# Optimization experiments

Measured on AMD Instinct MI355X. Metric: run time of the kernel, lower is better.

Reference implementation:

```python
import jax, jax.numpy as jnp
import numpy as np

HEADS = 16
ROPE_BASE = 10000.0


def _rope(x, cos, sin):
    # x: [B, H, L, hd]; rotate_half = [-x2, x1]
    x1, x2 = jnp.split(x, 2, axis=-1)
    rot = jnp.concatenate((-x2, x1), axis=-1)
    return x * cos + rot * sin


def setup_inputs() -> dict:
    key = jax.random.key(0)
    ks = jax.random.split(key, 8)
    B, L, D = 2, 2048, 1024
    s = 0.02
    inp = {
        "Q": jax.random.normal(ks[0], (B, L, D), jnp.float32),
        "K": jax.random.normal(ks[1], (B, L, D), jnp.float32),
        "V": jax.random.normal(ks[2], (B, L, D), jnp.float32),
        # Linear weights stored as [in, out] (transpose of torch's [out, in])
        "Wq": jax.random.normal(ks[3], (D, D), jnp.float32) * s,
        "Wk": jax.random.normal(ks[4], (D, D), jnp.float32) * s,
        "Wv": jax.random.normal(ks[5], (D, D), jnp.float32) * s,
        "Wo": jax.random.normal(ks[6], (D, D), jnp.float32) * s,
        "bq": jnp.zeros((D,), jnp.float32),
        "bk": jnp.zeros((D,), jnp.float32),
        "bv": jnp.zeros((D,), jnp.float32),
        "bo": jnp.zeros((D,), jnp.float32),
        # causal mask, 0 = masked, broadcast to [B,1,L,L]
        "mask": jnp.broadcast_to(jnp.tril(jnp.ones((L, L), jnp.int32))[None, None], (B, 1, L, L)),
    }
    return inp


def reference(Q, K, V, Wq, Wk, Wv, Wo, bq, bk, bv, bo, mask):
    B, L, D = Q.shape
    H = HEADS
    hd = D // H

    def proj(x, W, b):
        # [B,L,D] -> [B,H,L,hd]
        return (x @ W + b).reshape(B, -1, H, hd).transpose(0, 2, 1, 3)

    q = proj(Q, Wq, bq)
    k = proj(K, Wk, bk)
    v = proj(V, Wv, bv)

    # RoPE tables (deterministic constants)
    inv_freq = 1.0 / (ROPE_BASE ** (jnp.arange(0, hd, 2, dtype=jnp.float32) / hd))
    t = jnp.arange(L, dtype=jnp.float32)
    freqs = jnp.outer(t, inv_freq)              # [L, hd/2]
    emb = jnp.concatenate((freqs, freqs), -1)   # [L, hd]
    cos = jnp.cos(emb)[None, None]              # [1,1,L,hd]
    sin = jnp.sin(emb)[None, None]
    q = _rope(q, cos, sin)
    k = _rope(k, cos, sin)

    scale = jnp.sqrt(jnp.asarray(hd, q.dtype))
    scores = jnp.einsum('bhqd,bhkd->bhqk', q, k) / scale
    scores = jnp.where(mask == 0, jnp.asarray(-1e9, scores.dtype), scores)
    attn = jax.nn.softmax(scores, axis=-1)
    out = jnp.einsum('bhqk,bhkd->bhqd', attn, v)
    out = out.transpose(0, 2, 1, 3).reshape(B, L, D)
    return out @ Wo + bo
```

## Files before the change

kernel.cpp:

```cpp
#include <hip/hip_runtime.h>

typedef __attribute__((ext_vector_type(8))) short short8;
typedef __attribute__((ext_vector_type(4))) float f32x4;
typedef unsigned short u16;
typedef unsigned int u32;

#define MFMA_BF16(a, b, c) __builtin_amdgcn_mfma_f32_16x16x32_bf16((a), (b), (c), 0, 0, 0)

constexpr int D = 1024;
constexpr int L = 2048;
constexpr int NHEAD = 16;
constexpr int HD = 64;
constexpr float QLAMBDA = 0.125f * 1.44269504088896340736f;

__device__ __forceinline__ u16 f2bf(float f) {
  unsigned u = __builtin_bit_cast(unsigned, f);
  u = (u + 0x7fffu + ((u >> 16) & 1u)) >> 16;
  return (u16)u;
}

__device__ __forceinline__ short8 cvt8(f32x4 lo, f32x4 hi) {
  short8 r;
  r[0] = (short)f2bf(lo[0]); r[1] = (short)f2bf(lo[1]);
  r[2] = (short)f2bf(lo[2]); r[3] = (short)f2bf(lo[3]);
  r[4] = (short)f2bf(hi[0]); r[5] = (short)f2bf(hi[1]);
  r[6] = (short)f2bf(hi[2]); r[7] = (short)f2bf(hi[3]);
  return r;
}

__device__ __forceinline__ void gload16(const u16* src, u16* dst) {
  __builtin_amdgcn_global_load_lds(
      (const __attribute__((address_space(1))) u32*)(src),
      (__attribute__((address_space(3))) u32*)(dst), 16, 0, 0);
}

__global__ __launch_bounds__(256) void wt_trans_kernel(const float* W0, const float* W1,
                                                       const float* W2, const float* W3,
                                                       u16* out) {
  const float* W = blockIdx.z == 0 ? W0 : blockIdx.z == 1 ? W1 : blockIdx.z == 2 ? W2 : W3;
  u16* o = out + (size_t)blockIdx.z * D * D;
  __shared__ float t[32][33];
  int x = threadIdx.x & 31, y = threadIdx.x >> 5;
  int k0 = blockIdx.x * 32, n0 = blockIdx.y * 32;
#pragma unroll
  for (int i = 0; i < 4; i++) {
    int ky = y * 4 + i;
    t[ky][x] = W[(size_t)(k0 + ky) * D + n0 + x];
  }
  __syncthreads();
#pragma unroll
  for (int i = 0; i < 4; i++) {
    int ny = y * 4 + i;
    o[(size_t)(n0 + ny) * D + k0 + x] = f2bf(t[x][ny]);
  }
}

__global__ __launch_bounds__(256) void rope_tab_kernel(float* ct, float* st) {
  int t = blockIdx.x * 256 + threadIdx.x;
  int i = t & 31, pos = t >> 5;
  float invf = powf(10000.0f, -(float)i / 32.0f);
  float ang = (float)pos * invf;
  ct[t] = cosf(ang);
  st[t] = sinf(ang);
}

__global__ __launch_bounds__(256) void cvt_x_kernel(const float* Q, const float* K,
                                                    const float* V, u16* xb) {
  const float* src = blockIdx.y == 0 ? Q : blockIdx.y == 1 ? K : V;
  u16* dst = xb + (size_t)blockIdx.y * 4096 * D;
  int t = blockIdx.x * 256 + threadIdx.x;
  const float* p = src + (size_t)t * 8;
  f32x4 lo = *(const f32x4*)p;
  f32x4 hi = *(const f32x4*)(p + 4);
  *(short8*)(dst + (size_t)t * 8) = cvt8(lo, hi);
}


__global__ __launch_bounds__(256, 3) void proj_gemm_staged(
    const u16* xb, const u16* wT,
    const float* bq, const float* bk, const float* bv,
    const float* ct, const float* st,
    u16* qo, u16* ko, u16* vT) {
  int i = blockIdx.x;
  int swz = (i & 7) * 96 + (i >> 3);
  int z = swz >> 8;
  int bx = swz & 7;
  int by = (swz >> 3) & 31;

  const u16* A = xb + (size_t)z * 4096 * D;
  const u16* W = wT + (size_t)z * D * D;
  const float* bias = z == 0 ? bq : z == 1 ? bk : bv;

  int w = threadIdx.x >> 6, lane = threadIdx.x & 63;
  int r = lane & 15, c = lane >> 4;
  int wr = w >> 1, wc = w & 1;
  int m0 = by * 128 + wr * 64;
  int n0 = bx * 128 + wc * 64;

  __shared__ __align__(16) u16 lsA[2][4096];
  __shared__ __align__(16) u16 lsB[2][4096];

  const u16* aSrc[2];
  const u16* bSrc[2];
  int dstOff[2];
#pragma unroll
  for (int i2 = 0; i2 < 2; i2++) {
    int q0 = i2 * 256 + w * 64;
    int qq = q0 + lane;
    int t = qq >> 2;
    int gch = (qq & 3) ^ ((t >> 1) & 3);
    aSrc[i2] = A + (size_t)(by * 128 + t) * D + gch * 8;
    bSrc[i2] = W + (size_t)(bx * 128 + t) * D + gch * 8;
    dstOff[i2] = q0 * 8;
  }

  int aOff[4], bOff[4];
#pragma unroll
  for (int mi = 0; mi < 4; mi++) {
    int rowA = wr * 64 + mi * 16 + r;
    aOff[mi] = rowA * 32 + ((c ^ ((rowA >> 1) & 3)) << 3);
    int rowB = wc * 64 + mi * 16 + r;
    bOff[mi] = rowB * 32 + ((c ^ ((rowB >> 1) & 3)) << 3);
  }

  f32x4 acc[4][4];
#pragma unroll
  for (int mi = 0; mi < 4; mi++)
#pragma unroll
    for (int ni = 0; ni < 4; ni++) acc[mi][ni] = f32x4{0.f, 0.f, 0.f, 0.f};

#pragma unroll
  for (int i2 = 0; i2 < 2; i2++) {
    gload16(aSrc[i2], &lsA[0][dstOff[i2]]);
    gload16(bSrc[i2], &lsB[0][dstOff[i2]]);
  }

  auto compute = [&](const u16* pa, const u16* pb) {
    short8 af[4], bf[4];
#pragma unroll
    for (int mi = 0; mi < 4; mi++) af[mi] = *(const short8*)(pa + aOff[mi]);
#pragma unroll
    for (int ni = 0; ni < 4; ni++) bf[ni] = *(const short8*)(pb + bOff[ni]);
#pragma unroll
    for (int mi = 0; mi < 4; mi++)
#pragma unroll
      for (int ni = 0; ni < 4; ni++)
        acc[mi][ni] = MFMA_BF16(af[mi], bf[ni], acc[mi][ni]);
  };

  for (int kt = 0; kt < 31; kt++) {
    int cur = kt & 1;
    __syncthreads();
#pragma unroll
    for (int i2 = 0; i2 < 2; i2++) {
      gload16(aSrc[i2] + (kt + 1) * 32, &lsA[cur ^ 1][dstOff[i2]]);
      gload16(bSrc[i2] + (kt + 1) * 32, &lsB[cur ^ 1][dstOff[i2]]);
    }
    compute(lsA[cur], lsB[cur]);
  }
  __syncthreads();
  compute(lsA[1], lsB[1]);

  int h = n0 >> 6;
#pragma unroll
  for (int mi = 0; mi < 4; mi++) {
#pragma unroll
    for (int j = 0; j < 4; j++) {
      int grow = m0 + mi * 16 + c * 4 + j;
      int b = grow >> 11, ll = grow & 2047;
      if (z < 2) {
        u16* o = (z == 0) ? qo : ko;
        float lam = (z == 0) ? QLAMBDA : 1.0f;
        size_t dst = ((size_t)(b * NHEAD + h) * L + ll) * HD;
#pragma unroll
        for (int ni = 0; ni < 2; ni++) {
          int d = ni * 16 + r;
          float x1 = acc[mi][ni][j] + bias[n0 + d];
          float x2 = acc[mi][ni + 2][j] + bias[n0 + 32 + d];
          float cs = ct[ll * 32 + d], sn = st[ll * 32 + d];
          o[dst + d]      = f2bf((x1 * cs - x2 * sn) * lam);
          o[dst + d + 32] = f2bf((x2 * cs + x1 * sn) * lam);
        }
      } else {
#pragma unroll
        for (int ni = 0; ni < 4; ni++) {
          int d = ni * 16 + r;
          float val = acc[mi][ni][j] + bias[n0 + d];
          vT[((size_t)(b * NHEAD + h) * HD + d) * L + ll] = f2bf(val);
        }
      }
    }
  }
}

__global__ __launch_bounds__(256) void proj_gemm_f32(
    const float* Qf, const float* Kf, const float* Vf, const u16* wT,
    const float* bq, const float* bk, const float* bv,
    const float* ct, const float* st,
    u16* qo, u16* ko, u16* vT) {
  int i = blockIdx.x;
  int swz = (i & 7) * 96 + (i >> 3);
  int z = swz >> 8;
  int bx = swz & 7;
  int by = (swz >> 3) & 31;

  const u16* W = wT + (size_t)z * D * D;
  const float* bias = z == 0 ? bq : z == 1 ? bk : bv;

  int w = threadIdx.x >> 6, lane = threadIdx.x & 63;
  int r = lane & 15, c = lane >> 4;
  int wr = w >> 1, wc = w & 1;
  int m0 = by * 128 + wr * 64;
  int n0 = bx * 128 + wc * 64;

  const float* Af = z == 0 ? Qf : z == 1 ? Kf : Vf;
  const float* a0f = Af + (size_t)(m0 + r) * D + c * 8;
  const u16* b0 = W + (size_t)(n0 + r) * D + c * 8;

  f32x4 acc[4][4];
#pragma unroll
  for (int mi = 0; mi < 4; mi++)
#pragma unroll
    for (int ni = 0; ni < 4; ni++) acc[mi][ni] = f32x4{0.f, 0.f, 0.f, 0.f};

  for (int kk = 0; kk < D; kk += 32) {
    short8 af[4], bf[4];
#pragma unroll
    for (int mi = 0; mi < 4; mi++) {
      const float* ap = a0f + (size_t)mi * 16 * D;
      af[mi] = cvt8(*(const f32x4*)ap, *(const f32x4*)(ap + 4));
    }
#pragma unroll
    for (int ni = 0; ni < 4; ni++) bf[ni] = *(const short8*)(b0 + (size_t)ni * 16 * D);
#pragma unroll
    for (int mi = 0; mi < 4; mi++)
#pragma unroll
      for (int ni = 0; ni < 4; ni++)
        acc[mi][ni] = MFMA_BF16(af[mi], bf[ni], acc[mi][ni]);
    a0f += 32;
    b0 += 32;
  }

  int h = n0 >> 6;
#pragma unroll
  for (int mi = 0; mi < 4; mi++) {
#pragma unroll
    for (int j = 0; j < 4; j++) {
      int grow = m0 + mi * 16 + c * 4 + j;
      int b = grow >> 11, ll = grow & 2047;
      if (z < 2) {
        u16* o = (z == 0) ? qo : ko;
        float lam = (z == 0) ? QLAMBDA : 1.0f;
        size_t dst = ((size_t)(b * NHEAD + h) * L + ll) * HD;
#pragma unroll
        for (int ni = 0; ni < 2; ni++) {
          int d = ni * 16 + r;
          float x1 = acc[mi][ni][j] + bias[n0 + d];
          float x2 = acc[mi][ni + 2][j] + bias[n0 + 32 + d];
          float cs = ct[ll * 32 + d], sn = st[ll * 32 + d];
          o[dst + d]      = f2bf((x1 * cs - x2 * sn) * lam);
          o[dst + d + 32] = f2bf((x2 * cs + x1 * sn) * lam);
        }
      } else {
#pragma unroll
        for (int ni = 0; ni < 4; ni++) {
          int d = ni * 16 + r;
          float val = acc[mi][ni][j] + bias[n0 + d];
          vT[((size_t)(b * NHEAD + h) * HD + d) * L + ll] = f2bf(val);
        }
      }
    }
  }
}

__global__ __launch_bounds__(256) void attn_kernel(const u16* qg, const u16* kg,
                                                   const u16* vg, u16* O) {
  int i = blockIdx.x;
  int xcd = i & 7, j = i >> 3;
  int bh = xcd * 4 + (j & 3);
  int a = j >> 2;
  int qtA = a, qtB = 31 - a;

  int w = threadIdx.x >> 6, lane = threadIdx.x & 63;
  int r = lane & 15, c = lane >> 4;
  int qbA = qtA * 64 + w * 16;
  int qbB = qtB * 64 + w * 16;

  const u16* qp = qg + (size_t)bh * L * HD;
  const u16* kp = kg + (size_t)bh * L * HD;
  const u16* vp = vg + (size_t)bh * HD * L;

  __shared__ __align__(16) u16 kls[2][4096];
  __shared__ __align__(16) u16 vls[2][4096];
  __shared__ __align__(16) u16 plds[4][16][64];

  short8 aqA0 = *(const short8*)(qp + (size_t)(qbA + r) * HD + c * 8);
  short8 aqA1 = *(const short8*)(qp + (size_t)(qbA + r) * HD + 32 + c * 8);
  short8 aqB0 = *(const short8*)(qp + (size_t)(qbB + r) * HD + c * 8);
  short8 aqB1 = *(const short8*)(qp + (size_t)(qbB + r) * HD + 32 + c * 8);

  const short one_bf = (short)0x3F80;
  short8 ones = {one_bf, one_bf, one_bf, one_bf, one_bf, one_bf, one_bf, one_bf};

  f32x4 oA[4], oB[4];
  f32x4 sacA = f32x4{0.f, 0.f, 0.f, 0.f};
  f32x4 sacB = f32x4{0.f, 0.f, 0.f, 0.f};
#pragma unroll
  for (int n = 0; n < 4; n++) {
    oA[n] = f32x4{0.f, 0.f, 0.f, 0.f};
    oB[n] = f32x4{0.f, 0.f, 0.f, 0.f};
  }

  int nkt = qtB + 1;

#pragma unroll
  for (int rd = 0; rd < 2; rd++) {
    int q0 = (rd * 4 + w) << 6;
    int qq = q0 + lane;
    int row = qq >> 3;
    int gch = (qq & 7) ^ (row & 7);
    gload16(kp + (size_t)row * HD + gch * 8, &kls[0][q0 * 8]);
    gload16(vp + (size_t)row * L + gch * 8, &vls[0][q0 * 8]);
  }

  for (int kt = 0; kt < nkt; kt++) {
    int cur = kt & 1;
    __syncthreads();
    if (kt + 1 < nkt) {
      int kb2 = (kt + 1) * 64;
      const u16* kp2 = kp + (size_t)kb2 * HD;
      const u16* vp2 = vp + kb2;
#pragma unroll
      for (int rd = 0; rd < 2; rd++) {
        int q0 = (rd * 4 + w) << 6;
        int qq = q0 + lane;
        int row = qq >> 3;
        int gch = (qq & 7) ^ (row & 7);
        gload16(kp2 + (size_t)row * HD + gch * 8, &kls[cur ^ 1][q0 * 8]);
        gload16(vp2 + (size_t)row * L + gch * 8, &vls[cur ^ 1][q0 * 8]);
      }
    }
    const u16* kb_ = kls[cur];
    const u16* vb_ = vls[cur];
    int kbase = kt * 64;

    auto do_tile = [&](const short8& qf0, const short8& qf1, f32x4* o, f32x4& sac,
                       int qb, bool edge) {
      f32x4 S[4];
#pragma unroll
      for (int ks = 0; ks < 4; ks++) {
        int row = ks * 16 + r;
        short8 kf0 = *(const short8*)(kb_ + row * 64 + ((c ^ (row & 7)) << 3));
        short8 kf1 = *(const short8*)(kb_ + row * 64 + (((4 + c) ^ (row & 7)) << 3));
        S[ks] = f32x4{0.f, 0.f, 0.f, 0.f};
        S[ks] = MFMA_BF16(qf0, kf0, S[ks]);
        S[ks] = MFMA_BF16(qf1, kf1, S[ks]);
      }
#pragma unroll
      for (int j4 = 0; j4 < 4; j4++) {
        float p0 = exp2f(S[0][j4]);
        float p1 = exp2f(S[1][j4]);
        float p2 = exp2f(S[2][j4]);
        float p3 = exp2f(S[3][j4]);
        if (edge) {
          int qrow = qb + c * 4 + j4;
          if (kbase + r > qrow) p0 = 0.f;
          if (kbase + 16 + r > qrow) p1 = 0.f;
          if (kbase + 32 + r > qrow) p2 = 0.f;
          if (kbase + 48 + r > qrow) p3 = 0.f;
        }
        int prow = c * 4 + j4, xr = (prow & 7) << 3;
        plds[w][prow][(r) ^ xr]      = f2bf(p0);
        plds[w][prow][(16 + r) ^ xr] = f2bf(p1);
        plds[w][prow][(32 + r) ^ xr] = f2bf(p2);
        plds[w][prow][(48 + r) ^ xr] = f2bf(p3);
      }
      int xrr = (r & 7) << 3;
      short8 pa0 = *(const short8*)&plds[w][r][(c * 8) ^ xrr];
      short8 pa1 = *(const short8*)&plds[w][r][(32 + c * 8) ^ xrr];
      sac = MFMA_BF16(pa0, ones, sac);
      sac = MFMA_BF16(pa1, ones, sac);
#pragma unroll
      for (int n = 0; n < 4; n++) {
        int row = n * 16 + r;
        short8 vf0 = *(const short8*)(vb_ + row * 64 + ((c ^ (row & 7)) << 3));
        short8 vf1 = *(const short8*)(vb_ + row * 64 + (((4 + c) ^ (row & 7)) << 3));
        o[n] = MFMA_BF16(pa0, vf0, o[n]);
        o[n] = MFMA_BF16(pa1, vf1, o[n]);
      }
    };

    do_tile(aqB0, aqB1, oB, sacB, qbB, kt == nkt - 1);
    if (kt <= qtA) do_tile(aqA0, aqA1, oA, sacA, qbA, kt == qtA);
  }

  int b = bh >> 4, h = bh & 15;
#pragma unroll
  for (int j4 = 0; j4 < 4; j4++) {
    int qrowA = qbA + c * 4 + j4;
    int qrowB = qbB + c * 4 + j4;
    float invA = 1.0f / sacA[j4];
    float invB = 1.0f / sacB[j4];
#pragma unroll
    for (int n = 0; n < 4; n++) {
      O[((size_t)(b * L + qrowA)) * D + h * HD + n * 16 + r] = f2bf(oA[n][j4] * invA);
      O[((size_t)(b * L + qrowB)) * D + h * HD + n * 16 + r] = f2bf(oB[n][j4] * invB);
    }
  }
}

__global__ __launch_bounds__(256, 3) void oproj_gemm_staged(const u16* Ag, const u16* wT,
                                                            const float* bias, float* out) {
  int i = blockIdx.x;
  int swz = (i & 7) * 32 + (i >> 3);
  int bx = swz & 7, by = swz >> 3;

  int w = threadIdx.x >> 6, lane = threadIdx.x & 63;
  int r = lane & 15, c = lane >> 4;
  int wr = w >> 1, wc = w & 1;
  int m0 = by * 128 + wr * 64;
  int n0 = bx * 128 + wc * 64;

  __shared__ __align__(16) u16 lsA[2][4096];
  __shared__ __align__(16) u16 lsB[2][4096];

  const u16* aSrc[2];
  const u16* bSrc[2];
  int dstOff[2];
#pragma unroll
  for (int i2 = 0; i2 < 2; i2++) {
    int q0 = i2 * 256 + w * 64;
    int qq = q0 + lane;
    int t = qq >> 2;
    int gch = (qq & 3) ^ ((t >> 1) & 3);
    aSrc[i2] = Ag + (size_t)(by * 128 + t) * D + gch * 8;
    bSrc[i2] = wT + (size_t)(bx * 128 + t) * D + gch * 8;
    dstOff[i2] = q0 * 8;
  }

  int aOff[4], bOff[4];
#pragma unroll
  for (int mi = 0; mi < 4; mi++) {
    int rowA = wr * 64 + mi * 16 + r;
    aOff[mi] = rowA * 32 + ((c ^ ((rowA >> 1) & 3)) << 3);
    int rowB = wc * 64 + mi * 16 + r;
    bOff[mi] = rowB * 32 + ((c ^ ((rowB >> 1) & 3)) << 3);
  }

  f32x4 acc[4][4];
#pragma unroll
  for (int mi = 0; mi < 4; mi++)
#pragma unroll
    for (int ni = 0; ni < 4; ni++) acc[mi][ni] = f32x4{0.f, 0.f, 0.f, 0.f};

#pragma unroll
  for (int i2 = 0; i2 < 2; i2++) {
    gload16(aSrc[i2], &lsA[0][dstOff[i2]]);
    gload16(bSrc[i2], &lsB[0][dstOff[i2]]);
  }

  auto compute = [&](const u16* pa, const u16* pb) {
    short8 af[4], bf[4];
#pragma unroll
    for (int mi = 0; mi < 4; mi++) af[mi] = *(const short8*)(pa + aOff[mi]);
#pragma unroll
    for (int ni = 0; ni < 4; ni++) bf[ni] = *(const short8*)(pb + bOff[ni]);
#pragma unroll
    for (int mi = 0; mi < 4; mi++)
#pragma unroll
      for (int ni = 0; ni < 4; ni++)
        acc[mi][ni] = MFMA_BF16(af[mi], bf[ni], acc[mi][ni]);
  };

  for (int kt = 0; kt < 31; kt++) {
    int cur = kt & 1;
    __syncthreads();
#pragma unroll
    for (int i2 = 0; i2 < 2; i2++) {
      gload16(aSrc[i2] + (kt + 1) * 32, &lsA[cur ^ 1][dstOff[i2]]);
      gload16(bSrc[i2] + (kt + 1) * 32, &lsB[cur ^ 1][dstOff[i2]]);
    }
    compute(lsA[cur], lsB[cur]);
  }
  __syncthreads();
  compute(lsA[1], lsB[1]);

#pragma unroll
  for (int mi = 0; mi < 4; mi++)
#pragma unroll
    for (int j = 0; j < 4; j++) {
      int grow = m0 + mi * 16 + c * 4 + j;
#pragma unroll
      for (int ni = 0; ni < 4; ni++) {
        int gcol = n0 + ni * 16 + r;
        out[(size_t)grow * D + gcol] = acc[mi][ni][j] + bias[gcol];
      }
    }
}

extern "C" void kernel_launch(void* const* d_in, const int* in_sizes, int n_in,
                              void* d_out, int out_size, void* d_ws, size_t ws_size,
                              hipStream_t stream) {
  const float* Q = (const float*)d_in[0];
  const float* K = (const float*)d_in[1];
  const float* V = (const float*)d_in[2];
  const float* Wq = (const float*)d_in[3];
  const float* Wk = (const float*)d_in[4];
  const float* Wv = (const float*)d_in[5];
  const float* Wo = (const float*)d_in[6];
  const float* bq = (const float*)d_in[7];
  const float* bk = (const float*)d_in[8];
  const float* bv = (const float*)d_in[9];
  const float* bo = (const float*)d_in[10];
  float* out = (float*)d_out;

  char* ws = (char*)d_ws;
  u16* wT = (u16*)(ws);
  u16* woT = wT + (size_t)3 * 1024 * 1024;
  float* ct = (float*)(ws + 8388608);
  float* st = (float*)(ws + 8650752);
  u16* qbuf = (u16*)(ws + 8912896);
  u16* kbuf = (u16*)(ws + 17301504);
  u16* vbuf = (u16*)(ws + 25690112);
  u16* obuf = (u16*)(ws + 34078720);
  u16* xb = (u16*)(ws + 42467328);

  wt_trans_kernel<<<dim3(32, 32, 4), 256, 0, stream>>>(Wq, Wk, Wv, Wo, wT);
  rope_tab_kernel<<<dim3(256), 256, 0, stream>>>(ct, st);

  if (ws_size >= (size_t)67633152) {
    cvt_x_kernel<<<dim3(2048, 3), 256, 0, stream>>>(Q, K, V, xb);
    proj_gemm_staged<<<dim3(768), 256, 0, stream>>>(xb, wT, bq, bk, bv, ct, st,
                                                    qbuf, kbuf, vbuf);
  } else {
    proj_gemm_f32<<<dim3(768), 256, 0, stream>>>(Q, K, V, wT, bq, bk, bv, ct, st,
                                                 qbuf, kbuf, vbuf);
  }
  attn_kernel<<<dim3(512), 256, 0, stream>>>(qbuf, kbuf, vbuf, obuf);
  oproj_gemm_staged<<<dim3(256), 256, 0, stream>>>(obuf, woT, bo, out);
}
```

Baseline: 264.9 us.

## Merge prep kernels into one launch and interleave attention tile pair work

The weight transpose, RoPE table and input conversion kernels are combined into a single launch that dispatches on block index, which removes two launch gaps. In the attention kernel, the two query tiles that share each K/V tile are now computed together instead of through sequential lambda calls. K and V fragments are loaded once for both tiles, and the tiles' MFMA chains are interleaved for more instruction-level parallelism. The P staging buffer is doubled per wave, which uses more LDS and more registers and could lower occupancy.

New measurement: 269.6 us. Within noise of the previous version (+1.8%).

```diff
diff --git a/kernel.cpp b/kernel.cpp
--- a/kernel.cpp
+++ b/kernel.cpp
@@ -34,45 +34,48 @@
       (__attribute__((address_space(3))) u32*)(dst), 16, 0, 0);
 }
 
-__global__ __launch_bounds__(256) void wt_trans_kernel(const float* W0, const float* W1,
-                                                       const float* W2, const float* W3,
-                                                       u16* out) {
-  const float* W = blockIdx.z == 0 ? W0 : blockIdx.z == 1 ? W1 : blockIdx.z == 2 ? W2 : W3;
-  u16* o = out + (size_t)blockIdx.z * D * D;
-  __shared__ float t[32][33];
-  int x = threadIdx.x & 31, y = threadIdx.x >> 5;
-  int k0 = blockIdx.x * 32, n0 = blockIdx.y * 32;
-#pragma unroll
-  for (int i = 0; i < 4; i++) {
-    int ky = y * 4 + i;
-    t[ky][x] = W[(size_t)(k0 + ky) * D + n0 + x];
-  }
-  __syncthreads();
-#pragma unroll
-  for (int i = 0; i < 4; i++) {
-    int ny = y * 4 + i;
-    o[(size_t)(n0 + ny) * D + k0 + x] = f2bf(t[x][ny]);
-  }
-}
-
-__global__ __launch_bounds__(256) void rope_tab_kernel(float* ct, float* st) {
-  int t = blockIdx.x * 256 + threadIdx.x;
-  int i = t & 31, pos = t >> 5;
-  float invf = powf(10000.0f, -(float)i / 32.0f);
-  float ang = (float)pos * invf;
-  ct[t] = cosf(ang);
-  st[t] = sinf(ang);
-}
-
-__global__ __launch_bounds__(256) void cvt_x_kernel(const float* Q, const float* K,
-                                                    const float* V, u16* xb) {
-  const float* src = blockIdx.y == 0 ? Q : blockIdx.y == 1 ? K : V;
-  u16* dst = xb + (size_t)blockIdx.y * 4096 * D;
-  int t = blockIdx.x * 256 + threadIdx.x;
-  const float* p = src + (size_t)t * 8;
-  f32x4 lo = *(const f32x4*)p;
-  f32x4 hi = *(const f32x4*)(p + 4);
-  *(short8*)(dst + (size_t)t * 8) = cvt8(lo, hi);
+template <bool DO_CVT>
+__global__ __launch_bounds__(256) void prep_kernel(
+    const float* W0, const float* W1, const float* W2, const float* W3, u16* wTout,
+    float* ct, float* st,
+    const float* Q, const float* K, const float* V, u16* xb) {
+  int i = blockIdx.x;
+  if (i < 4096) {
+    int z = i >> 10, bx = i & 31, by = (i >> 5) & 31;
+    const float* W = z == 0 ? W0 : z == 1 ? W1 : z == 2 ? W2 : W3;
+    u16* o = wTout + (size_t)z * D * D;
+    __shared__ float t[32][33];
+    int x = threadIdx.x & 31, y = threadIdx.x >> 5;
+    int k0 = bx * 32, n0 = by * 32;
+#pragma unroll
+    for (int q = 0; q < 4; q++) {
+      int ky = y * 4 + q;
+      t[ky][x] = W[(size_t)(k0 + ky) * D + n0 + x];
+    }
+    __syncthreads();
+#pragma unroll
+    for (int q = 0; q < 4; q++) {
+      int ny = y * 4 + q;
+      o[(size_t)(n0 + ny) * D + k0 + x] = f2bf(t[x][ny]);
+    }
+  } else if (i < 4352) {
+    int t = (i - 4096) * 256 + threadIdx.x;
+    int ii = t & 31, pos = t >> 5;
+    float invf = powf(10000.0f, -(float)ii / 32.0f);
+    float ang = (float)pos * invf;
+    ct[t] = cosf(ang);
+    st[t] = sinf(ang);
+  } else if constexpr (DO_CVT) {
+    int j = i - 4352;
+    int zz = j / 2048, bx = j - zz * 2048;
+    const float* src = zz == 0 ? Q : zz == 1 ? K : V;
+    u16* dst = xb + (size_t)zz * 4096 * D;
+    int t = bx * 256 + threadIdx.x;
+    const float* p = src + (size_t)t * 8;
+    f32x4 lo = *(const f32x4*)p;
+    f32x4 hi = *(const f32x4*)(p + 4);
+    *(short8*)(dst + (size_t)t * 8) = cvt8(lo, hi);
+  }
 }
 
 
@@ -292,7 +295,7 @@
 
   __shared__ __align__(16) u16 kls[2][4096];
   __shared__ __align__(16) u16 vls[2][4096];
-  __shared__ __align__(16) u16 plds[4][16][64];
+  __shared__ __align__(16) u16 plds[4][2][16][64];
 
   short8 aqA0 = *(const short8*)(qp + (size_t)(qbA + r) * HD + c * 8);
   short8 aqA1 = *(const short8*)(qp + (size_t)(qbA + r) * HD + 32 + c * 8);
@@ -343,55 +346,91 @@
     const u16* kb_ = kls[cur];
     const u16* vb_ = vls[cur];
     int kbase = kt * 64;
-
-    auto do_tile = [&](const short8& qf0, const short8& qf1, f32x4* o, f32x4& sac,
-                       int qb, bool edge) {
-      f32x4 S[4];
-#pragma unroll
-      for (int ks = 0; ks < 4; ks++) {
-        int row = ks * 16 + r;
-        short8 kf0 = *(const short8*)(kb_ + row * 64 + ((c ^ (row & 7)) << 3));
-        short8 kf1 = *(const short8*)(kb_ + row * 64 + (((4 + c) ^ (row & 7)) << 3));
-        S[ks] = f32x4{0.f, 0.f, 0.f, 0.f};
-        S[ks] = MFMA_BF16(qf0, kf0, S[ks]);
-        S[ks] = MFMA_BF16(qf1, kf1, S[ks]);
-      }
+    bool actA = (kt <= qtA);
+
+    f32x4 SB[4], SA[4];
+#pragma unroll
+    for (int ks = 0; ks < 4; ks++) {
+      int row = ks * 16 + r;
+      short8 kf0 = *(const short8*)(kb_ + row * 64 + ((c ^ (row & 7)) << 3));
+      short8 kf1 = *(const short8*)(kb_ + row * 64 + (((4 + c) ^ (row & 7)) << 3));
+      SB[ks] = f32x4{0.f, 0.f, 0.f, 0.f};
+      SB[ks] = MFMA_BF16(aqB0, kf0, SB[ks]);
+      SB[ks] = MFMA_BF16(aqB1, kf1, SB[ks]);
+      if (actA) {
+        SA[ks] = f32x4{0.f, 0.f, 0.f, 0.f};
+        SA[ks] = MFMA_BF16(aqA0, kf0, SA[ks]);
+        SA[ks] = MFMA_BF16(aqA1, kf1, SA[ks]);
+      }
+    }
+
+    bool edgeB = (kt == nkt - 1);
+#pragma unroll
+    for (int j4 = 0; j4 < 4; j4++) {
+      float p0 = exp2f(SB[0][j4]);
+      float p1 = exp2f(SB[1][j4]);
+      float p2 = exp2f(SB[2][j4]);
+      float p3 = exp2f(SB[3][j4]);
+      if (edgeB) {
+        int qrow = qbB + c * 4 + j4;
+        if (kbase + r > qrow) p0 = 0.f;
+        if (kbase + 16 + r > qrow) p1 = 0.f;
+        if (kbase + 32 + r > qrow) p2 = 0.f;
+        if (kbase + 48 + r > qrow) p3 = 0.f;
+      }
+      int prow = c * 4 + j4, xr = (prow & 7) << 3;
+      plds[w][0][prow][(r) ^ xr]      = f2bf(p0);
+      plds[w][0][prow][(16 + r) ^ xr] = f2bf(p1);
+      plds[w][0][prow][(32 + r) ^ xr] = f2bf(p2);
+      plds[w][0][prow][(48 + r) ^ xr] = f2bf(p3);
+    }
+    if (actA) {
+      bool edgeA = (kt == qtA);
 #pragma unroll
       for (int j4 = 0; j4 < 4; j4++) {
-        float p0 = exp2f(S[0][j4]);
-        float p1 = exp2f(S[1][j4]);
-        float p2 = exp2f(S[2][j4]);
-        float p3 = exp2f(S[3][j4]);
-        if (edge) {
-          int qrow = qb + c * 4 + j4;
+        float p0 = exp2f(SA[0][j4]);
+        float p1 = exp2f(SA[1][j4]);
+        float p2 = exp2f(SA[2][j4]);
+        float p3 = exp2f(SA[3][j4]);
+        if (edgeA) {
+          int qrow = qbA + c * 4 + j4;
           if (kbase + r > qrow) p0 = 0.f;
           if (kbase + 16 + r > qrow) p1 = 0.f;
           if (kbase + 32 + r > qrow) p2 = 0.f;
           if (kbase + 48 + r > qrow) p3 = 0.f;
         }
         int prow = c * 4 + j4, xr = (prow & 7) << 3;
-        plds[w][prow][(r) ^ xr]      = f2bf(p0);
-        plds[w][prow][(16 + r) ^ xr] = f2bf(p1);
-        plds[w][prow][(32 + r) ^ xr] = f2bf(p2);
-        plds[w][prow][(48 + r) ^ xr] = f2bf(p3);
-      }
-      int xrr = (r & 7) << 3;
-      short8 pa0 = *(const short8*)&plds[w][r][(c * 8) ^ xrr];
-      short8 pa1 = *(const short8*)&plds[w][r][(32 + c * 8) ^ xrr];
-      sac = MFMA_BF16(pa0, ones, sac);
-      sac = MFMA_BF16(pa1, ones, sac);
-#pragma unroll
-      for (int n = 0; n < 4; n++) {
-        int row = n * 16 + r;
-        short8 vf0 = *(const short8*)(vb_ + row * 64 + ((c ^ (row & 7)) << 3));
-        short8 vf1 = *(const short8*)(vb_ + row * 64 + (((4 + c) ^ (row & 7)) << 3));
-        o[n] = MFMA_BF16(pa0, vf0, o[n]);
-        o[n] = MFMA_BF16(pa1, vf1, o[n]);
-      }
-    };
-
-    do_tile(aqB0, aqB1, oB, sacB, qbB, kt == nkt - 1);
-    if (kt <= qtA) do_tile(aqA0, aqA1, oA, sacA, qbA, kt == qtA);
+        plds[w][1][prow][(r) ^ xr]      = f2bf(p0);
+        plds[w][1][prow][(16 + r) ^ xr] = f2bf(p1);
+        plds[w][1][prow][(32 + r) ^ xr] = f2bf(p2);
+        plds[w][1][prow][(48 + r) ^ xr] = f2bf(p3);
+      }
+    }
+
+    int xrr = (r & 7) << 3;
+    short8 paB0 = *(const short8*)&plds[w][0][r][(c * 8) ^ xrr];
+    short8 paB1 = *(const short8*)&plds[w][0][r][(32 + c * 8) ^ xrr];
+    sacB = MFMA_BF16(paB0, ones, sacB);
+    sacB = MFMA_BF16(paB1, ones, sacB);
+    short8 paA0, paA1;
+    if (actA) {
+      paA0 = *(const short8*)&plds[w][1][r][(c * 8) ^ xrr];
+      paA1 = *(const short8*)&plds[w][1][r][(32 + c * 8) ^ xrr];
+      sacA = MFMA_BF16(paA0, ones, sacA);
+      sacA = MFMA_BF16(paA1, ones, sacA);
+    }
+#pragma unroll
+    for (int n = 0; n < 4; n++) {
+      int row = n * 16 + r;
+      short8 vf0 = *(const short8*)(vb_ + row * 64 + ((c ^ (row & 7)) << 3));
+      short8 vf1 = *(const short8*)(vb_ + row * 64 + (((4 + c) ^ (row & 7)) << 3));
+      oB[n] = MFMA_BF16(paB0, vf0, oB[n]);
+      oB[n] = MFMA_BF16(paB1, vf1, oB[n]);
+      if (actA) {
+        oA[n] = MFMA_BF16(paA0, vf0, oA[n]);
+        oA[n] = MFMA_BF16(paA1, vf1, oA[n]);
+      }
+    }
   }
 
   int b = bh >> 4, h = bh & 15;
@@ -525,14 +564,14 @@
   u16* obuf = (u16*)(ws + 34078720);
   u16* xb = (u16*)(ws + 42467328);
 
-  wt_trans_kernel<<<dim3(32, 32, 4), 256, 0, stream>>>(Wq, Wk, Wv, Wo, wT);
-  rope_tab_kernel<<<dim3(256), 256, 0, stream>>>(ct, st);
-
   if (ws_size >= (size_t)67633152) {
-    cvt_x_kernel<<<dim3(2048, 3), 256, 0, stream>>>(Q, K, V, xb);
+    prep_kernel<true><<<dim3(10496), 256, 0, stream>>>(Wq, Wk, Wv, Wo, wT, ct, st,
+                                                       Q, K, V, xb);
     proj_gemm_staged<<<dim3(768), 256, 0, stream>>>(xb, wT, bq, bk, bv, ct, st,
                                                     qbuf, kbuf, vbuf);
   } else {
+    prep_kernel<false><<<dim3(4352), 256, 0, stream>>>(Wq, Wk, Wv, Wo, wT, ct, st,
+                                                       Q, K, V, xb);
     proj_gemm_f32<<<dim3(768), 256, 0, stream>>>(Q, K, V, wT, bq, bk, bv, ct, st,
                                                  qbuf, kbuf, vbuf);
   }
```
